# Kernel optimization log

Measured on AMD Instinct MI355X. Metric: run time of the kernel, lower is better.

## Reference

```python
import jax, jax.numpy as jnp
import numpy as np

N_NODES = 50000
N_EDGES = 1600000
N_GRAPHS = 512
HID = 32
NEG_SLOPE = 0.2  # PyG GATConv default leaky_relu slope
EPS = 1e-16      # PyG softmax denominator epsilon


def setup_inputs() -> dict:
    key = jax.random.key(0)
    ks = jax.random.split(key, 12)
    x = jax.random.normal(ks[0], (N_NODES, 12), jnp.float32)
    edge_index = jax.random.randint(ks[1], (2, N_EDGES), 0, N_NODES)
    edge_attr = jax.random.normal(ks[2], (N_EDGES, 3), jnp.float32)
    batch = jnp.sort(jax.random.randint(ks[3], (N_NODES,), 0, N_GRAPHS))
    g = lambda k, shp: jax.random.normal(k, shp, jnp.float32) * (1.0 / np.sqrt(shp[0]))
    return {
        "x": x, "edge_index": edge_index, "edge_attr": edge_attr, "batch": batch,
        "W": g(ks[4], (12, HID)),
        "att_src": g(ks[5], (HID,)), "att_dst": g(ks[6], (HID,)),
        "W_edge": g(ks[7], (3, HID)), "att_edge": g(ks[8], (HID,)),
        "bias": jnp.zeros((HID,), jnp.float32),
        "W_gate": g(ks[9], (HID, 1)), "b_gate": jnp.zeros((1,), jnp.float32),
        "W_out": g(ks[10], (HID, 1)), "b_out": jnp.zeros((1,), jnp.float32),
    }


def reference(x, edge_index, edge_attr, batch, W, att_src, att_dst, W_edge,
              att_edge, bias, W_gate, b_gate, W_out, b_out):
    N = x.shape[0]
    src, dst = edge_index[0], edge_index[1]

    # --- add self loops, edge_attr fill_value='mean' (mean of incoming edge attrs per node)
    deg = jax.ops.segment_sum(jnp.ones_like(edge_attr[:, 0]), dst, num_segments=N)
    loop_attr = jax.ops.segment_sum(edge_attr, dst, num_segments=N) / jnp.maximum(deg, 1.0)[:, None]
    loop = jnp.arange(N, dtype=src.dtype)
    src_f = jnp.concatenate([src, loop])
    dst_f = jnp.concatenate([dst, loop])
    ea = jnp.concatenate([edge_attr, loop_attr], axis=0)  # [E+N, 3]

    # --- GATConv (heads=1)
    h = x @ W                       # [N, HID]
    a_src = h @ att_src             # [N]
    a_dst = h @ att_dst             # [N]
    a_edge = (ea @ W_edge) @ att_edge  # [E+N]
    alpha = jax.nn.leaky_relu(a_src[src_f] + a_dst[dst_f] + a_edge, NEG_SLOPE)
    # segment softmax over destination neighborhoods
    m = jax.ops.segment_max(alpha, dst_f, num_segments=N)
    e = jnp.exp(alpha - m[dst_f])
    z = jax.ops.segment_sum(e, dst_f, num_segments=N)
    alpha = e / (z[dst_f] + EPS)
    out = jax.ops.segment_sum(h[src_f] * alpha[:, None], dst_f, num_segments=N) + bias

    out = jax.nn.relu(out)  # dropout is identity in eval mode

    # --- GlobalAttention pooling: gate = softmax(Linear(out), batch)
    gate = (out @ W_gate + b_gate)[:, 0]  # [N]
    gm = jax.ops.segment_max(gate, batch, num_segments=N_GRAPHS)
    ge = jnp.exp(gate - gm[batch])
    gz = jax.ops.segment_sum(ge, batch, num_segments=N_GRAPHS)
    gate = ge / (gz[batch] + EPS)
    pooled = jax.ops.segment_sum(out * gate[:, None], batch, num_segments=N_GRAPHS)  # [G, HID]

    return jax.nn.sigmoid(pooled @ W_out + b_out)  # [G, 1]
```

## Files before the change

kernel.cpp:

```cpp
#include <hip/hip_runtime.h>
#include <hip/hip_fp16.h>
#include <math.h>

#define N_NODES 50000
#define N_EDGES 1600000
#define N_GRAPHS 512
#define HID 32
#define NEG_SLOPE 0.2f
#define SM_EPS 1e-16f
#define PAD 80
#define NBIN 511
#define BIN_W 98
#define BIN_CAP 3800
#define EPT 10
#define PART_BLOCKS 625
#define MAXG 8

__global__ __launch_bounds__(256) void k_part_node(const int* __restrict__ ei,
                                                   const float* __restrict__ ea,
                                                   const float* __restrict__ W_edge,
                                                   const float* __restrict__ att_edge,
                                                   const float* __restrict__ x,
                                                   const float* __restrict__ W,
                                                   const float* __restrict__ att_src,
                                                   const float* __restrict__ att_dst,
                                                   uint2* __restrict__ part,
                                                   int* __restrict__ pcur,
                                                   __half2* __restrict__ h2,
                                                   float* __restrict__ a_src,
                                                   float* __restrict__ a_dst) {
    __shared__ float sv[3];
    __shared__ float sW[12 * 32], sas[32], sad[32];
    __shared__ int lcnt[NBIN], lcur[NBIN];
    int t = threadIdx.x;
    if (t < 3) {
        float v = 0.f;
        for (int j = 0; j < 32; ++j) v += W_edge[t * 32 + j] * att_edge[j];
        sv[t] = v;
    }
    for (int i = t; i < 12 * 32; i += 256) sW[i] = W[i];
    if (t < 32) { sas[t] = att_src[t]; sad[t] = att_dst[t]; }
    for (int i = t; i < NBIN; i += 256) lcnt[i] = 0;
    __syncthreads();

    uint2 r[EPT];
    int bin[EPT];
    int ebase = blockIdx.x * (256 * EPT) + t;
#pragma unroll
    for (int i = 0; i < EPT; ++i) {
        int e = ebase + i * 256;
        int s = ei[e];
        int d = ei[N_EDGES + e];
        float aev = ea[e * 3 + 0] * sv[0] + ea[e * 3 + 1] * sv[1] + ea[e * 3 + 2] * sv[2];
        r[i] = make_uint2((unsigned)d | ((unsigned)s << 16), __float_as_uint(aev));
        bin[i] = d / BIN_W;
        atomicAdd(&lcnt[bin[i]], 1);
    }
    __syncthreads();
    for (int i = t; i < NBIN; i += 256) lcur[i] = atomicAdd(pcur + i, lcnt[i]);
    __syncthreads();
#pragma unroll
    for (int i = 0; i < EPT; ++i) {
        int pos = atomicAdd(&lcur[bin[i]], 1);
        if (pos < BIN_CAP) part[(size_t)bin[i] * BIN_CAP + pos] = r[i];
    }

    int n = blockIdx.x * 80 + t;
    if (t < 80 && n < N_NODES) {
        float xv[12];
#pragma unroll
        for (int j = 0; j < 12; ++j) xv[j] = x[n * 12 + j];
        float hv[32];
        float as = 0.f, ad = 0.f;
#pragma unroll
        for (int k = 0; k < 32; ++k) {
            float acc = 0.f;
#pragma unroll
            for (int j = 0; j < 12; ++j) acc += xv[j] * sW[j * 32 + k];
            hv[k] = acc;
            as += acc * sas[k];
            ad += acc * sad[k];
        }
        a_src[n] = as;
        a_dst[n] = ad;
        __half2 hp[16];
#pragma unroll
        for (int k = 0; k < 16; ++k) hp[k] = __floats2half2_rn(hv[2 * k], hv[2 * k + 1]);
        uint4* dst = (uint4*)(h2 + (size_t)n * 16);
        const uint4* srcp = (const uint4*)hp;
#pragma unroll
        for (int k = 0; k < 4; ++k) dst[k] = srcp[k];
    }
}

__global__ __launch_bounds__(1024) void k_asm_gather(const uint2* __restrict__ part,
                                                     const int* __restrict__ pcur,
                                                     const __half2* __restrict__ h2,
                                                     const float* __restrict__ a_src,
                                                     const float* __restrict__ a_dst,
                                                     const float* __restrict__ bias,
                                                     const float* __restrict__ W_gate,
                                                     const float* __restrict__ b_gate,
                                                     const int* __restrict__ batch,
                                                     float* __restrict__ Sg,
                                                     float* __restrict__ gzg) {
    int b = blockIdx.x;
    int lo = b * BIN_W;
    if (lo >= N_NODES) return;
    int hi = lo + BIN_W; if (hi > N_NODES) hi = N_NODES;
    int nrow = hi - lo;
    __shared__ int lcur[BIN_W];
    __shared__ unsigned lbuck[BIN_W * PAD];
    __shared__ float S_local[MAXG][32];
    __shared__ float gz_local[MAXG];
    __shared__ int sgf, sgl;
    int t = threadIdx.x;
    if (t < BIN_W) lcur[t] = 0;
    if (t < MAXG * 32) S_local[t >> 5][t & 31] = 0.f;
    if (t < MAXG) gz_local[t] = 0.f;
    if (t == 0) { sgf = batch[lo]; sgl = batch[hi - 1]; }
    __syncthreads();
    int gfirst = sgf;

    int cnt = pcur[b]; if (cnt > BIN_CAP) cnt = BIN_CAP;
    const uint2* p = part + (size_t)b * BIN_CAP;
    for (int i = t; i < cnt; i += 1024) {
        uint2 r = p[i];
        int li = (int)(r.x & 0xFFFF) - lo;
        unsigned s = r.x >> 16;
        unsigned short hb = __half_as_ushort(__float2half_rn(__uint_as_float(r.y)));
        int pos = atomicAdd(&lcur[li], 1);
        if (pos < PAD) lbuck[li * PAD + pos] = s | ((unsigned)hb << 16);
    }
    __syncthreads();

    int l = t & 63, wl = t >> 6;
    int es = l >> 2;
    int cg = l & 3;
    float bg0 = b_gate[0];

    for (int li = wl; li < nrow; li += 16) {
        int n = lo + li;
        int deg_full = lcur[li];
        int degc = deg_full < PAD ? deg_full : PAD;
        float adst_n = a_dst[n];
        const unsigned* row = lbuck + li * PAD;

        float c0 = 0.f, c1 = 0.f, c2 = 0.f, c3 = 0.f, c4 = 0.f, c5 = 0.f, c6 = 0.f, c7 = 0.f;
        float wsum = 0.f, aevsum = 0.f;
        int j = es;
        for (; j + 16 < degc; j += 32) {
            unsigned p0 = row[j], p1 = row[j + 16];
            int s0 = p0 & 0xFFFF, s1 = p1 & 0xFFFF;
            float aev0 = __half2float(__ushort_as_half((unsigned short)(p0 >> 16)));
            float aev1 = __half2float(__ushort_as_half((unsigned short)(p1 >> 16)));
            float as0 = a_src[s0], as1 = a_src[s1];
            const uint4 u0 = *(const uint4*)(h2 + (size_t)s0 * 16 + cg * 4);
            const uint4 u1 = *(const uint4*)(h2 + (size_t)s1 * 16 + cg * 4);
            float a0 = as0 + adst_n + aev0; a0 = a0 > 0.f ? a0 : NEG_SLOPE * a0;
            float a1 = as1 + adst_n + aev1; a1 = a1 > 0.f ? a1 : NEG_SLOPE * a1;
            float w0 = __expf(a0), w1 = __expf(a1);
            wsum += w0 + w1; aevsum += aev0 + aev1;
            float2 f;
            f = __half22float2(*(const __half2*)&u0.x); c0 += w0 * f.x; c1 += w0 * f.y;
            f = __half22float2(*(const __half2*)&u0.y); c2 += w0 * f.x; c3 += w0 * f.y;
            f = __half22float2(*(const __half2*)&u0.z); c4 += w0 * f.x; c5 += w0 * f.y;
            f = __half22float2(*(const __half2*)&u0.w); c6 += w0 * f.x; c7 += w0 * f.y;
            f = __half22float2(*(const __half2*)&u1.x); c0 += w1 * f.x; c1 += w1 * f.y;
            f = __half22float2(*(const __half2*)&u1.y); c2 += w1 * f.x; c3 += w1 * f.y;
            f = __half22float2(*(const __half2*)&u1.z); c4 += w1 * f.x; c5 += w1 * f.y;
            f = __half22float2(*(const __half2*)&u1.w); c6 += w1 * f.x; c7 += w1 * f.y;
        }
        if (j < degc) {
            unsigned p0 = row[j];
            int s0 = p0 & 0xFFFF;
            float aev0 = __half2float(__ushort_as_half((unsigned short)(p0 >> 16)));
            float a0 = a_src[s0] + adst_n + aev0; a0 = a0 > 0.f ? a0 : NEG_SLOPE * a0;
            float w0 = __expf(a0);
            const uint4 u0 = *(const uint4*)(h2 + (size_t)s0 * 16 + cg * 4);
            wsum += w0; aevsum += aev0;
            float2 f;
            f = __half22float2(*(const __half2*)&u0.x); c0 += w0 * f.x; c1 += w0 * f.y;
            f = __half22float2(*(const __half2*)&u0.y); c2 += w0 * f.x; c3 += w0 * f.y;
            f = __half22float2(*(const __half2*)&u0.z); c4 += w0 * f.x; c5 += w0 * f.y;
            f = __half22float2(*(const __half2*)&u0.w); c6 += w0 * f.x; c7 += w0 * f.y;
        }

#pragma unroll
        for (int m = 4; m <= 32; m <<= 1) {
            c0 += __shfl_xor(c0, m); c1 += __shfl_xor(c1, m);
            c2 += __shfl_xor(c2, m); c3 += __shfl_xor(c3, m);
            c4 += __shfl_xor(c4, m); c5 += __shfl_xor(c5, m);
            c6 += __shfl_xor(c6, m); c7 += __shfl_xor(c7, m);
            wsum += __shfl_xor(wsum, m); aevsum += __shfl_xor(aevsum, m);
        }

        float dgm = deg_full > 1 ? (float)deg_full : 1.f;
        float al = a_src[n] + adst_n + aevsum / dgm;
        al = al > 0.f ? al : NEG_SLOPE * al;
        float el = __expf(al);
        float zi = 1.f / (wsum + el + SM_EPS);

        if (es == 0) {
            const uint4 un = *(const uint4*)(h2 + (size_t)n * 16 + cg * 4);
            float hn[8];
            float2 f;
            f = __half22float2(*(const __half2*)&un.x); hn[0] = f.x; hn[1] = f.y;
            f = __half22float2(*(const __half2*)&un.y); hn[2] = f.x; hn[3] = f.y;
            f = __half22float2(*(const __half2*)&un.z); hn[4] = f.x; hn[5] = f.y;
            f = __half22float2(*(const __half2*)&un.w); hn[6] = f.x; hn[7] = f.y;
            const float4 bva = *(const float4*)(bias + cg * 8);
            const float4 bvb = *(const float4*)(bias + cg * 8 + 4);
            float v[8];
            v[0] = (c0 + el * hn[0]) * zi + bva.x;
            v[1] = (c1 + el * hn[1]) * zi + bva.y;
            v[2] = (c2 + el * hn[2]) * zi + bva.z;
            v[3] = (c3 + el * hn[3]) * zi + bva.w;
            v[4] = (c4 + el * hn[4]) * zi + bvb.x;
            v[5] = (c5 + el * hn[5]) * zi + bvb.y;
            v[6] = (c6 + el * hn[6]) * zi + bvb.z;
            v[7] = (c7 + el * hn[7]) * zi + bvb.w;
#pragma unroll
            for (int k = 0; k < 8; ++k) v[k] = v[k] > 0.f ? v[k] : 0.f;
            const float4 wga = *(const float4*)(W_gate + cg * 8);
            const float4 wgb = *(const float4*)(W_gate + cg * 8 + 4);
            float g = v[0] * wga.x + v[1] * wga.y + v[2] * wga.z + v[3] * wga.w
                    + v[4] * wgb.x + v[5] * wgb.y + v[6] * wgb.z + v[7] * wgb.w;
            g += __shfl_xor(g, 1);
            g += __shfl_xor(g, 2);
            float gen = __expf(g + bg0);
            int gi = batch[n] - gfirst; gi = gi < MAXG - 1 ? gi : MAXG - 1;
#pragma unroll
            for (int k = 0; k < 8; ++k) atomicAdd(&S_local[gi][cg * 8 + k], gen * v[k]);
            if (cg == 0) atomicAdd(&gz_local[gi], gen);
        }
    }
    __syncthreads();

    int ngr = sgl - gfirst + 1; if (ngr > MAXG) ngr = MAXG;
    for (int i = t; i < ngr * 33; i += 1024) {
        int q = i / 33, c = i % 33;
        if (c < 32) atomicAdd(&Sg[(size_t)(gfirst + q) * 32 + c], S_local[q][c]);
        else atomicAdd(&gzg[gfirst + q], gz_local[q]);
    }
}

__global__ __launch_bounds__(256) void k_out(const float* __restrict__ Sg,
                                             const float* __restrict__ gzg,
                                             const float* __restrict__ W_out,
                                             const float* __restrict__ b_out,
                                             float* __restrict__ out) {
    int g = blockIdx.x * blockDim.x + threadIdx.x;
    if (g >= N_GRAPHS) return;
    float zi = 1.f / (gzg[g] + SM_EPS);
    float acc = b_out[0];
#pragma unroll
    for (int k = 0; k < 32; ++k) acc += Sg[(size_t)g * 32 + k] * zi * W_out[k];
    out[g] = 1.f / (1.f + __expf(-acc));
}

extern "C" void kernel_launch(void* const* d_in, const int* in_sizes, int n_in,
                              void* d_out, int out_size, void* d_ws, size_t ws_size,
                              hipStream_t stream) {
    const float* x        = (const float*)d_in[0];
    const int*   ei       = (const int*)  d_in[1];
    const float* ea       = (const float*)d_in[2];
    const int*   batch    = (const int*)  d_in[3];
    const float* W        = (const float*)d_in[4];
    const float* att_src  = (const float*)d_in[5];
    const float* att_dst  = (const float*)d_in[6];
    const float* W_edge   = (const float*)d_in[7];
    const float* att_edge = (const float*)d_in[8];
    const float* bias     = (const float*)d_in[9];
    const float* W_gate   = (const float*)d_in[10];
    const float* b_gate   = (const float*)d_in[11];
    const float* W_out    = (const float*)d_in[12];
    const float* b_out    = (const float*)d_in[13];
    float* out = (float*)d_out;

    char* wsb = (char*)d_ws;
    uint2*    part_  = (uint2*)wsb;
    __half2*  h2     = (__half2*)(part_ + (size_t)NBIN * BIN_CAP);
    float*    a_src  = (float*)(h2 + (size_t)16 * N_NODES);
    float*    a_dst  = a_src + N_NODES;
    float*    Sg     = a_dst + N_NODES;
    float*    gzg    = Sg + (size_t)N_GRAPHS * 32;
    int*      pcur   = (int*)(gzg + N_GRAPHS);

    size_t zero_bytes = ((size_t)N_GRAPHS * 33 + NBIN) * sizeof(float);
    hipMemsetAsync(Sg, 0, zero_bytes, stream);

    const int B = 256;
    k_part_node<<<PART_BLOCKS, B, 0, stream>>>(ei, ea, W_edge, att_edge, x, W, att_src,
                                               att_dst, part_, pcur, h2, a_src, a_dst);
    k_asm_gather<<<NBIN, 1024, 0, stream>>>(part_, pcur, h2, a_src, a_dst, bias,
                                            W_gate, b_gate, batch, Sg, gzg);
    k_out<<<(N_GRAPHS + B - 1) / B, B, 0, stream>>>(Sg, gzg, W_out, b_out, out);
}
```

Before: 173.0 us.

## Precompute per-edge attention weights once per edge in a separate shared-memory pass

Adds a pass after bucketing in which each edge is handled by a single thread. That thread computes its leaky-relu and exp weight and stores the weight as fp16 in place of the edge attribute. Row sums and attribute sums are accumulated with shared atomics, and per-row self-loop terms are precomputed. The main gather loop no longer repeats the a_src load and the exp across the four channel-group lanes that cover each edge. In exchange it adds an extra pass, shared-memory atomics and fp16 rounding of the weights, with the weights clamped at 60000 before conversion.

Result: slower. 187.8 us (+8.5%).

```diff
diff --git a/kernel.cpp b/kernel.cpp
--- a/kernel.cpp
+++ b/kernel.cpp
@@ -111,11 +111,16 @@
     int nrow = hi - lo;
     __shared__ int lcur[BIN_W];
     __shared__ unsigned lbuck[BIN_W * PAD];
+    __shared__ float wsum_l[BIN_W], aev_l[BIN_W], as_row[BIN_W], ad_row[BIN_W];
+    __shared__ float el_row[BIN_W], zi_row[BIN_W];
     __shared__ float S_local[MAXG][32];
     __shared__ float gz_local[MAXG];
     __shared__ int sgf, sgl;
     int t = threadIdx.x;
-    if (t < BIN_W) lcur[t] = 0;
+    if (t < BIN_W) {
+        lcur[t] = 0; wsum_l[t] = 0.f; aev_l[t] = 0.f;
+        as_row[t] = a_src[lo + t]; ad_row[t] = a_dst[lo + t];
+    }
     if (t < MAXG * 32) S_local[t >> 5][t & 31] = 0.f;
     if (t < MAXG) gz_local[t] = 0.f;
     if (t == 0) { sgf = batch[lo]; sgl = batch[hi - 1]; }
@@ -134,6 +139,35 @@
     }
     __syncthreads();
 
+    for (int idx = t; idx < nrow * PAD; idx += 1024) {
+        int li = idx / PAD, pos = idx - li * PAD;
+        int dc = lcur[li]; if (dc > PAD) dc = PAD;
+        if (pos < dc) {
+            unsigned e = lbuck[idx];
+            int s = e & 0xFFFF;
+            float aev = __half2float(__ushort_as_half((unsigned short)(e >> 16)));
+            float a = a_src[s] + ad_row[li] + aev;
+            a = a > 0.f ? a : NEG_SLOPE * a;
+            float w = __expf(a);
+            w = w < 60000.f ? w : 60000.f;
+            unsigned short wh = __half_as_ushort(__float2half_rn(w));
+            lbuck[idx] = (unsigned)s | ((unsigned)wh << 16);
+            atomicAdd(&wsum_l[li], __half2float(__ushort_as_half(wh)));
+            atomicAdd(&aev_l[li], aev);
+        }
+    }
+    __syncthreads();
+    if (t < nrow) {
+        int dg = lcur[t];
+        float dgm = dg > 1 ? (float)dg : 1.f;
+        float al = as_row[t] + ad_row[t] + aev_l[t] / dgm;
+        al = al > 0.f ? al : NEG_SLOPE * al;
+        float el = __expf(al);
+        el_row[t] = el;
+        zi_row[t] = 1.f / (wsum_l[t] + el + SM_EPS);
+    }
+    __syncthreads();
+
     int l = t & 63, wl = t >> 6;
     int es = l >> 2;
     int cg = l & 3;
@@ -141,26 +175,18 @@
 
     for (int li = wl; li < nrow; li += 16) {
         int n = lo + li;
-        int deg_full = lcur[li];
-        int degc = deg_full < PAD ? deg_full : PAD;
-        float adst_n = a_dst[n];
+        int degc = lcur[li]; degc = degc < PAD ? degc : PAD;
         const unsigned* row = lbuck + li * PAD;
 
         float c0 = 0.f, c1 = 0.f, c2 = 0.f, c3 = 0.f, c4 = 0.f, c5 = 0.f, c6 = 0.f, c7 = 0.f;
-        float wsum = 0.f, aevsum = 0.f;
         int j = es;
         for (; j + 16 < degc; j += 32) {
             unsigned p0 = row[j], p1 = row[j + 16];
             int s0 = p0 & 0xFFFF, s1 = p1 & 0xFFFF;
-            float aev0 = __half2float(__ushort_as_half((unsigned short)(p0 >> 16)));
-            float aev1 = __half2float(__ushort_as_half((unsigned short)(p1 >> 16)));
-            float as0 = a_src[s0], as1 = a_src[s1];
+            float w0 = __half2float(__ushort_as_half((unsigned short)(p0 >> 16)));
+            float w1 = __half2float(__ushort_as_half((unsigned short)(p1 >> 16)));
             const uint4 u0 = *(const uint4*)(h2 + (size_t)s0 * 16 + cg * 4);
             const uint4 u1 = *(const uint4*)(h2 + (size_t)s1 * 16 + cg * 4);
-            float a0 = as0 + adst_n + aev0; a0 = a0 > 0.f ? a0 : NEG_SLOPE * a0;
-            float a1 = as1 + adst_n + aev1; a1 = a1 > 0.f ? a1 : NEG_SLOPE * a1;
-            float w0 = __expf(a0), w1 = __expf(a1);
-            wsum += w0 + w1; aevsum += aev0 + aev1;
             float2 f;
             f = __half22float2(*(const __half2*)&u0.x); c0 += w0 * f.x; c1 += w0 * f.y;
             f = __half22float2(*(const __half2*)&u0.y); c2 += w0 * f.x; c3 += w0 * f.y;
@@ -174,11 +200,8 @@
         if (j < degc) {
             unsigned p0 = row[j];
             int s0 = p0 & 0xFFFF;
-            float aev0 = __half2float(__ushort_as_half((unsigned short)(p0 >> 16)));
-            float a0 = a_src[s0] + adst_n + aev0; a0 = a0 > 0.f ? a0 : NEG_SLOPE * a0;
-            float w0 = __expf(a0);
+            float w0 = __half2float(__ushort_as_half((unsigned short)(p0 >> 16)));
             const uint4 u0 = *(const uint4*)(h2 + (size_t)s0 * 16 + cg * 4);
-            wsum += w0; aevsum += aev0;
             float2 f;
             f = __half22float2(*(const __half2*)&u0.x); c0 += w0 * f.x; c1 += w0 * f.y;
             f = __half22float2(*(const __half2*)&u0.y); c2 += w0 * f.x; c3 += w0 * f.y;
@@ -192,14 +215,10 @@
             c2 += __shfl_xor(c2, m); c3 += __shfl_xor(c3, m);
             c4 += __shfl_xor(c4, m); c5 += __shfl_xor(c5, m);
             c6 += __shfl_xor(c6, m); c7 += __shfl_xor(c7, m);
-            wsum += __shfl_xor(wsum, m); aevsum += __shfl_xor(aevsum, m);
-        }
-
-        float dgm = deg_full > 1 ? (float)deg_full : 1.f;
-        float al = a_src[n] + adst_n + aevsum / dgm;
-        al = al > 0.f ? al : NEG_SLOPE * al;
-        float el = __expf(al);
-        float zi = 1.f / (wsum + el + SM_EPS);
+        }
+
+        float el = el_row[li];
+        float zi = zi_row[li];
 
         if (es == 0) {
             const uint4 un = *(const uint4*)(h2 + (size_t)n * 16 + cg * 4);
```
